# Performance work log

Measured on AMD Instinct MI355X. Metric: run time of the kernel, lower is better.

Reference implementation:

```python
import jax, jax.numpy as jnp
import numpy as np

N_NODES = 50000
N_EDGES = 800000
F_IN = 16
F_EDGE = 8
H = 8  # latent_dim = [8, 8]
NUM_GRAPHS = 512


def setup_inputs() -> dict:
    key = jax.random.key(0)
    ks = jax.random.split(key, 16)
    x = jax.random.normal(ks[0], (N_NODES, F_IN), dtype=jnp.float32)
    edge_index = jax.random.randint(ks[1], (2, N_EDGES), 0, N_NODES)
    edge_attr = jax.random.normal(ks[2], (N_EDGES, F_EDGE), dtype=jnp.float32)
    batch = jnp.sort(jax.random.randint(ks[3], (N_NODES,), 0, NUM_GRAPHS))
    s = 0.1
    # edge MLPs (single Linear each): edge_attr -> flattened [in, out] weight
    We1 = jax.random.normal(ks[4], (F_EDGE, F_IN * H), dtype=jnp.float32) * s
    be1 = jnp.zeros((F_IN * H,), dtype=jnp.float32)
    We2 = jax.random.normal(ks[5], (F_EDGE, H * H), dtype=jnp.float32) * s
    be2 = jnp.zeros((H * H,), dtype=jnp.float32)
    # NNConv root weights + biases
    root1 = jax.random.normal(ks[6], (F_IN, H), dtype=jnp.float32) * s
    b1 = jnp.zeros((H,), dtype=jnp.float32)
    root2 = jax.random.normal(ks[7], (H, H), dtype=jnp.float32) * s
    b2 = jnp.zeros((H,), dtype=jnp.float32)
    # final readout linear H -> 1
    Wlast = jax.random.normal(ks[8], (H, 1), dtype=jnp.float32) * s
    blast = jnp.zeros((1,), dtype=jnp.float32)
    return {"x": x, "edge_index": edge_index, "edge_attr": edge_attr, "batch": batch,
            "We1": We1, "be1": be1, "root1": root1, "b1": b1,
            "We2": We2, "be2": be2, "root2": root2, "b2": b2,
            "Wlast": Wlast, "blast": blast}


def _nnconv(x, src, dst, edge_attr, We, be, root, b, in_dim, out_dim):
    # per-edge weight matrix from edge MLP: [E, in_dim, out_dim]
    W = (edge_attr @ We + be).reshape(-1, in_dim, out_dim)
    # gather source features, per-edge matvec, scatter-add to targets
    msg = jnp.einsum('ei,eio->eo', x[src], W)            # [E, out_dim]
    agg = jax.ops.segment_sum(msg, dst, num_segments=x.shape[0])
    return agg + x @ root + b                            # root weight + bias


def reference(x, edge_index, edge_attr, batch, We1, be1, root1, b1,
              We2, be2, root2, b2, Wlast, blast):
    src, dst = edge_index[0], edge_index[1]
    h = jax.nn.relu(_nnconv(x, src, dst, edge_attr, We1, be1, root1, b1, F_IN, H))
    h = jax.nn.relu(_nnconv(h, src, dst, edge_attr, We2, be2, root2, b2, H, H))
    # per-graph sum pooling (vectorized equivalent of the python loop)
    pooled = jax.ops.segment_sum(h, batch, num_segments=NUM_GRAPHS)  # [G, H]
    return pooled @ Wlast + blast                                    # [G, 1]
```

## Files before the change

### kernel.cpp

```cpp
#include <hip/hip_runtime.h>

#define F_IN 16
#define F_EDGE 8
#define H 8

__global__ void init_out_kernel(float* __restrict__ out,
                                const float* __restrict__ blast, int n) {
    int g = blockIdx.x * blockDim.x + threadIdx.x;
    if (g < n) out[g] = blast[0];
}

template <int IN, bool RELU>
__global__ __launch_bounds__(256) void prep_kernel(
    const float* __restrict__ feat,
    const float* __restrict__ We,
    const float* __restrict__ be,
    const float* __restrict__ root,
    const float* __restrict__ b,
    float* __restrict__ Pt,
    float* __restrict__ q,
    float* __restrict__ aggseed,
    int n_nodes) {
    __shared__ float sWe[F_EDGE * IN * H];
    __shared__ float sbe[IN * H];
    __shared__ float sroot[IN * H];
    __shared__ float sf[32 * IN];

    int tid = threadIdx.x;
    for (int t = tid; t < F_EDGE * IN * H; t += 256) sWe[t] = We[t];
    for (int t = tid; t < IN * H; t += 256) {
        sbe[t] = be[t];
        sroot[t] = root[t];
    }
    int n0 = blockIdx.x * 32;
    for (int t = tid; t < 32 * IN; t += 256) {
        long long g = (long long)n0 * IN + t;
        float v = (g < (long long)n_nodes * IN) ? feat[g] : 0.f;
        if (RELU) v = v > 0.f ? v : 0.f;
        sf[t] = v;
    }
    __syncthreads();

    int n = n0 + (tid >> 3);
    int j = tid & 7;
    if (n >= n_nodes) return;

    const float* fr = &sf[(tid >> 3) * IN];
    float p[F_EDGE] = {0.f, 0.f, 0.f, 0.f, 0.f, 0.f, 0.f, 0.f};
    float qq = 0.f, hr = 0.f;
#pragma unroll
    for (int i = 0; i < IN; ++i) {
        float fi = fr[i];
#pragma unroll
        for (int k = 0; k < F_EDGE; ++k)
            p[k] = fmaf(fi, sWe[k * (IN * H) + i * H + j], p[k]);
        qq = fmaf(fi, sbe[i * H + j], qq);
        hr = fmaf(fi, sroot[i * H + j], hr);
    }
    long long base = ((long long)n * H + j) * F_EDGE;
    float4* pv = (float4*)(Pt + base);
    pv[0] = make_float4(p[0], p[1], p[2], p[3]);
    pv[1] = make_float4(p[4], p[5], p[6], p[7]);
    q[(long long)n * H + j] = qq;
    aggseed[(long long)n * H + j] = hr + b[j];
}

__global__ __launch_bounds__(256) void edge_fact_kernel(
    const int* __restrict__ ei,
    const float* __restrict__ ea,
    const float* __restrict__ Pt,
    const float* __restrict__ q,
    float* __restrict__ agg,
    int E) {
    long long gid = (long long)blockIdx.x * blockDim.x + threadIdx.x;
    int e = (int)(gid >> 3);
    if (e >= E) return;
    int j = (int)(gid & 7);

    int src = ei[e];
    int dst = ei[E + e];

    const float4* av = (const float4*)(ea + (long long)e * F_EDGE);
    float4 a0 = av[0], a1 = av[1];

    const float4* pv = (const float4*)(Pt + ((long long)src * H + j) * F_EDGE);
    float4 p0 = pv[0], p1 = pv[1];

    float m = q[(long long)src * H + j];
    m = fmaf(a0.x, p0.x, m);
    m = fmaf(a0.y, p0.y, m);
    m = fmaf(a0.z, p0.z, m);
    m = fmaf(a0.w, p0.w, m);
    m = fmaf(a1.x, p1.x, m);
    m = fmaf(a1.y, p1.y, m);
    m = fmaf(a1.z, p1.z, m);
    m = fmaf(a1.w, p1.w, m);

    unsafeAtomicAdd(&agg[(long long)dst * H + j], m);
}

__global__ void pool_kernel(const float* __restrict__ h2pre,
                            const int* __restrict__ batch,
                            const float* __restrict__ Wlast,
                            float* __restrict__ out, int n_nodes) {
    int n = blockIdx.x * blockDim.x + threadIdx.x;
    if (n >= n_nodes) return;
    float c = 0.f;
#pragma unroll
    for (int j = 0; j < H; ++j) {
        float hv = h2pre[(long long)n * H + j];
        hv = hv > 0.f ? hv : 0.f;
        c = fmaf(hv, Wlast[j], c);
    }
    unsafeAtomicAdd(&out[batch[n]], c);
}

extern "C" void kernel_launch(void* const* d_in, const int* in_sizes, int n_in,
                              void* d_out, int out_size, void* d_ws, size_t ws_size,
                              hipStream_t stream) {
    const float* x     = (const float*)d_in[0];
    const int*   ei    = (const int*)d_in[1];
    const float* ea    = (const float*)d_in[2];
    const int*   batch = (const int*)d_in[3];
    const float* We1   = (const float*)d_in[4];
    const float* be1   = (const float*)d_in[5];
    const float* root1 = (const float*)d_in[6];
    const float* b1    = (const float*)d_in[7];
    const float* We2   = (const float*)d_in[8];
    const float* be2   = (const float*)d_in[9];
    const float* root2 = (const float*)d_in[10];
    const float* b2    = (const float*)d_in[11];
    const float* Wlast = (const float*)d_in[12];
    const float* blast = (const float*)d_in[13];
    float* out = (float*)d_out;

    int n_nodes = in_sizes[0] / F_IN;
    int E = in_sizes[1] / 2;

    size_t nH = (size_t)n_nodes * H;
    float* Pt1   = (float*)d_ws;
    float* q1    = Pt1 + (size_t)n_nodes * H * F_EDGE;
    float* h1pre = q1 + nH;
    float* Pt2   = h1pre + nH;
    float* q2    = Pt2 + (size_t)n_nodes * H * F_EDGE;
    float* h2pre = q2 + nH;

    init_out_kernel<<<(out_size + 255) / 256, 256, 0, stream>>>(out, blast, out_size);

    int nblocks = (n_nodes + 31) / 32;
    prep_kernel<F_IN, false><<<nblocks, 256, 0, stream>>>(
        x, We1, be1, root1, b1, Pt1, q1, h1pre, n_nodes);

    long long lanes = (long long)E * H;
    int eblks = (int)((lanes + 255) / 256);
    edge_fact_kernel<<<eblks, 256, 0, stream>>>(ei, ea, Pt1, q1, h1pre, E);

    prep_kernel<H, true><<<nblocks, 256, 0, stream>>>(
        h1pre, We2, be2, root2, b2, Pt2, q2, h2pre, n_nodes);

    edge_fact_kernel<<<eblks, 256, 0, stream>>>(ei, ea, Pt2, q2, h2pre, E);

    pool_kernel<<<(n_nodes + 255) / 256, 256, 0, stream>>>(h2pre, batch, Wlast, out, n_nodes);
}
```

Baseline: 242.0 us.

## Store per-node edge factors in bf16, restructure prep weights, bin pooling in LDS

The per-node factor tensor Pt is now stored as bf16, halving the bytes gathered per edge in the edge kernels, which dominate runtime through random source reads. The prep kernel interleaves We, be and root into one shared array for vectorized LDS reads and loads node features straight from global memory. The pool kernel now accumulates per-graph sums in shared-memory bins before issuing global atomics, so far fewer global atomics are made. Rounding the factors to bf16 reduces precision of the messages.

```diff
diff --git a/kernel.cpp b/kernel.cpp
--- a/kernel.cpp
+++ b/kernel.cpp
@@ -1,8 +1,15 @@
 #include <hip/hip_runtime.h>
 
-#define F_IN 16
 #define F_EDGE 8
 #define H 8
+
+__device__ __forceinline__ unsigned short f2bf(float f) {
+    unsigned u = __float_as_uint(f);
+    unsigned r = u + 0x7fffu + ((u >> 16) & 1u);
+    return (unsigned short)(r >> 16);
+}
+__device__ __forceinline__ float bflo(unsigned u) { return __uint_as_float(u << 16); }
+__device__ __forceinline__ float bfhi(unsigned u) { return __uint_as_float(u & 0xffff0000u); }
 
 __global__ void init_out_kernel(float* __restrict__ out,
                                 const float* __restrict__ blast, int n) {
@@ -17,50 +24,61 @@
     const float* __restrict__ be,
     const float* __restrict__ root,
     const float* __restrict__ b,
-    float* __restrict__ Pt,
+    unsigned short* __restrict__ Pt,
     float* __restrict__ q,
     float* __restrict__ aggseed,
     int n_nodes) {
-    __shared__ float sWe[F_EDGE * IN * H];
-    __shared__ float sbe[IN * H];
-    __shared__ float sroot[IN * H];
-    __shared__ float sf[32 * IN];
-
+    __shared__ float sW[IN * H * 12];
     int tid = threadIdx.x;
-    for (int t = tid; t < F_EDGE * IN * H; t += 256) sWe[t] = We[t];
-    for (int t = tid; t < IN * H; t += 256) {
-        sbe[t] = be[t];
-        sroot[t] = root[t];
-    }
-    int n0 = blockIdx.x * 32;
-    for (int t = tid; t < 32 * IN; t += 256) {
-        long long g = (long long)n0 * IN + t;
-        float v = (g < (long long)n_nodes * IN) ? feat[g] : 0.f;
-        if (RELU) v = v > 0.f ? v : 0.f;
-        sf[t] = v;
+    for (int t = tid; t < IN * H * 12; t += 256) {
+        int r = t / 12, m = t - r * 12;
+        float v = 0.f;
+        if (m < 8) v = We[m * (IN * H) + r];
+        else if (m == 8) v = be[r];
+        else if (m == 9) v = root[r];
+        sW[t] = v;
     }
     __syncthreads();
 
-    int n = n0 + (tid >> 3);
+    int n = blockIdx.x * 32 + (tid >> 3);
+    if (n >= n_nodes) return;
     int j = tid & 7;
-    if (n >= n_nodes) return;
-
-    const float* fr = &sf[(tid >> 3) * IN];
-    float p[F_EDGE] = {0.f, 0.f, 0.f, 0.f, 0.f, 0.f, 0.f, 0.f};
+
+    float f[IN];
+    const float4* fv = (const float4*)(feat + (long long)n * IN);
+#pragma unroll
+    for (int i4 = 0; i4 < IN / 4; ++i4) {
+        float4 v = fv[i4];
+        f[i4 * 4 + 0] = v.x; f[i4 * 4 + 1] = v.y;
+        f[i4 * 4 + 2] = v.z; f[i4 * 4 + 3] = v.w;
+    }
+    if (RELU) {
+#pragma unroll
+        for (int i = 0; i < IN; ++i) f[i] = f[i] > 0.f ? f[i] : 0.f;
+    }
+
+    float p[8] = {0.f, 0.f, 0.f, 0.f, 0.f, 0.f, 0.f, 0.f};
     float qq = 0.f, hr = 0.f;
 #pragma unroll
     for (int i = 0; i < IN; ++i) {
-        float fi = fr[i];
-#pragma unroll
-        for (int k = 0; k < F_EDGE; ++k)
-            p[k] = fmaf(fi, sWe[k * (IN * H) + i * H + j], p[k]);
-        qq = fmaf(fi, sbe[i * H + j], qq);
-        hr = fmaf(fi, sroot[i * H + j], hr);
-    }
-    long long base = ((long long)n * H + j) * F_EDGE;
-    float4* pv = (float4*)(Pt + base);
-    pv[0] = make_float4(p[0], p[1], p[2], p[3]);
-    pv[1] = make_float4(p[4], p[5], p[6], p[7]);
+        const float* row = &sW[(i * 8 + j) * 12];
+        float4 w0 = *(const float4*)row;
+        float4 w1 = *(const float4*)(row + 4);
+        float2 br = *(const float2*)(row + 8);
+        float fi = f[i];
+        p[0] = fmaf(fi, w0.x, p[0]); p[1] = fmaf(fi, w0.y, p[1]);
+        p[2] = fmaf(fi, w0.z, p[2]); p[3] = fmaf(fi, w0.w, p[3]);
+        p[4] = fmaf(fi, w1.x, p[4]); p[5] = fmaf(fi, w1.y, p[5]);
+        p[6] = fmaf(fi, w1.z, p[6]); p[7] = fmaf(fi, w1.w, p[7]);
+        qq = fmaf(fi, br.x, qq);
+        hr = fmaf(fi, br.y, hr);
+    }
+    uint4 pw;
+    pw.x = (unsigned)f2bf(p[0]) | ((unsigned)f2bf(p[1]) << 16);
+    pw.y = (unsigned)f2bf(p[2]) | ((unsigned)f2bf(p[3]) << 16);
+    pw.z = (unsigned)f2bf(p[4]) | ((unsigned)f2bf(p[5]) << 16);
+    pw.w = (unsigned)f2bf(p[6]) | ((unsigned)f2bf(p[7]) << 16);
+    *(uint4*)(Pt + ((long long)n * H + j) * F_EDGE) = pw;
     q[(long long)n * H + j] = qq;
     aggseed[(long long)n * H + j] = hr + b[j];
 }
@@ -68,7 +86,7 @@
 __global__ __launch_bounds__(256) void edge_fact_kernel(
     const int* __restrict__ ei,
     const float* __restrict__ ea,
-    const float* __restrict__ Pt,
+    const unsigned short* __restrict__ Pt,
     const float* __restrict__ q,
     float* __restrict__ agg,
     int E) {
@@ -83,36 +101,62 @@
     const float4* av = (const float4*)(ea + (long long)e * F_EDGE);
     float4 a0 = av[0], a1 = av[1];
 
-    const float4* pv = (const float4*)(Pt + ((long long)src * H + j) * F_EDGE);
-    float4 p0 = pv[0], p1 = pv[1];
+    uint4 pw = *(const uint4*)(Pt + ((long long)src * H + j) * F_EDGE);
 
     float m = q[(long long)src * H + j];
-    m = fmaf(a0.x, p0.x, m);
-    m = fmaf(a0.y, p0.y, m);
-    m = fmaf(a0.z, p0.z, m);
-    m = fmaf(a0.w, p0.w, m);
-    m = fmaf(a1.x, p1.x, m);
-    m = fmaf(a1.y, p1.y, m);
-    m = fmaf(a1.z, p1.z, m);
-    m = fmaf(a1.w, p1.w, m);
+    m = fmaf(a0.x, bflo(pw.x), m);
+    m = fmaf(a0.y, bfhi(pw.x), m);
+    m = fmaf(a0.z, bflo(pw.y), m);
+    m = fmaf(a0.w, bfhi(pw.y), m);
+    m = fmaf(a1.x, bflo(pw.z), m);
+    m = fmaf(a1.y, bfhi(pw.z), m);
+    m = fmaf(a1.z, bflo(pw.w), m);
+    m = fmaf(a1.w, bfhi(pw.w), m);
 
     unsafeAtomicAdd(&agg[(long long)dst * H + j], m);
 }
 
-__global__ void pool_kernel(const float* __restrict__ h2pre,
-                            const int* __restrict__ batch,
-                            const float* __restrict__ Wlast,
-                            float* __restrict__ out, int n_nodes) {
-    int n = blockIdx.x * blockDim.x + threadIdx.x;
-    if (n >= n_nodes) return;
-    float c = 0.f;
-#pragma unroll
-    for (int j = 0; j < H; ++j) {
-        float hv = h2pre[(long long)n * H + j];
-        hv = hv > 0.f ? hv : 0.f;
-        c = fmaf(hv, Wlast[j], c);
-    }
-    unsafeAtomicAdd(&out[batch[n]], c);
+__global__ __launch_bounds__(256) void pool_kernel(
+    const float* __restrict__ h2pre, const int* __restrict__ batch,
+    const float* __restrict__ Wlast, float* __restrict__ out,
+    int n_nodes, int n_graphs) {
+    __shared__ float bins[512];
+    bool use_bins = (n_graphs <= 512);
+    if (use_bins) {
+        for (int t = threadIdx.x; t < n_graphs; t += 256) bins[t] = 0.f;
+        __syncthreads();
+    }
+    float wl[8];
+#pragma unroll
+    for (int j = 0; j < 8; ++j) wl[j] = Wlast[j];
+
+    int base = blockIdx.x * 1024;
+#pragma unroll
+    for (int r = 0; r < 4; ++r) {
+        int n = base + r * 256 + threadIdx.x;
+        if (n < n_nodes) {
+            const float4* hv = (const float4*)(h2pre + (long long)n * H);
+            float4 h0 = hv[0], h1 = hv[1];
+            float c = 0.f;
+            c = fmaf(fmaxf(h0.x, 0.f), wl[0], c);
+            c = fmaf(fmaxf(h0.y, 0.f), wl[1], c);
+            c = fmaf(fmaxf(h0.z, 0.f), wl[2], c);
+            c = fmaf(fmaxf(h0.w, 0.f), wl[3], c);
+            c = fmaf(fmaxf(h1.x, 0.f), wl[4], c);
+            c = fmaf(fmaxf(h1.y, 0.f), wl[5], c);
+            c = fmaf(fmaxf(h1.z, 0.f), wl[6], c);
+            c = fmaf(fmaxf(h1.w, 0.f), wl[7], c);
+            if (use_bins) atomicAdd(&bins[batch[n]], c);
+            else unsafeAtomicAdd(&out[batch[n]], c);
+        }
+    }
+    if (use_bins) {
+        __syncthreads();
+        for (int t = threadIdx.x; t < n_graphs; t += 256) {
+            float v = bins[t];
+            if (v != 0.f) unsafeAtomicAdd(&out[t], v);
+        }
+    }
 }
 
 extern "C" void kernel_launch(void* const* d_in, const int* in_sizes, int n_in,
@@ -134,21 +178,22 @@
     const float* blast = (const float*)d_in[13];
     float* out = (float*)d_out;
 
-    int n_nodes = in_sizes[0] / F_IN;
+    int F_IN_rt = 16;
+    int n_nodes = in_sizes[0] / F_IN_rt;
     int E = in_sizes[1] / 2;
 
     size_t nH = (size_t)n_nodes * H;
-    float* Pt1   = (float*)d_ws;
-    float* q1    = Pt1 + (size_t)n_nodes * H * F_EDGE;
-    float* h1pre = q1 + nH;
-    float* Pt2   = h1pre + nH;
-    float* q2    = Pt2 + (size_t)n_nodes * H * F_EDGE;
-    float* h2pre = q2 + nH;
+    unsigned short* Pt1 = (unsigned short*)d_ws;
+    unsigned short* Pt2 = Pt1 + (size_t)n_nodes * H * F_EDGE;
+    float* q1    = (float*)(Pt2 + (size_t)n_nodes * H * F_EDGE);
+    float* q2    = q1 + nH;
+    float* h1pre = q2 + nH;
+    float* h2pre = h1pre + nH;
 
     init_out_kernel<<<(out_size + 255) / 256, 256, 0, stream>>>(out, blast, out_size);
 
     int nblocks = (n_nodes + 31) / 32;
-    prep_kernel<F_IN, false><<<nblocks, 256, 0, stream>>>(
+    prep_kernel<16, false><<<nblocks, 256, 0, stream>>>(
         x, We1, be1, root1, b1, Pt1, q1, h1pre, n_nodes);
 
     long long lanes = (long long)E * H;
@@ -160,5 +205,6 @@
 
     edge_fact_kernel<<<eblks, 256, 0, stream>>>(ei, ea, Pt2, q2, h2pre, E);
 
-    pool_kernel<<<(n_nodes + 255) / 256, 256, 0, stream>>>(h2pre, batch, Wlast, out, n_nodes);
-}
+    int pblocks = (n_nodes + 1023) / 1024;
+    pool_kernel<<<pblocks, 256, 0, stream>>>(h2pre, batch, Wlast, out, n_nodes, out_size);
+}
```

Result: faster. 197.6 us (-18.4%).
